# Optimization experiments

Hardware: AMD Instinct MI355X
Metric: run time of the kernel (lower is better)

The kernel has to match this reference:

```python
import jax, jax.numpy as jnp
import numpy as np

B, M, R = 1024, 2048, 8192  # batch of states, metabolites, reactions
SPARSITY = 0.002            # ~4 nonzero substrates / products per reaction


def setup_inputs() -> dict:
    key = jax.random.key(0)
    k1, k2, k3, k4, k5, k6 = jax.random.split(key, 6)
    # concentrations must be strictly positive (log used in power-law eval)
    conc = jax.random.uniform(k1, (B, M), minval=1e-3, maxval=1.0, dtype=jnp.float32)
    # sparse kinetic-order (exponent) matrix: ~4 substrates/reaction, order 1 or 2
    e_mask = jax.random.bernoulli(k2, SPARSITY, (M, R))
    E = jnp.where(e_mask, jax.random.randint(k3, (M, R), 1, 3), 0).astype(jnp.int32)
    # sparse stoichiometry matrix with coefficients in {-2,-1,1,2}
    s_mask = jax.random.bernoulli(k4, SPARSITY, (M, R))
    s_raw = jax.random.randint(k5, (M, R), 0, 4)
    s_val = jnp.where(s_raw < 2, s_raw - 2, s_raw - 1)  # {-2,-1,1,2}
    S = jnp.where(s_mask, s_val, 0).astype(jnp.int32)
    # per-reaction rate constants (the learned ParameterDict)
    k = jax.random.uniform(k6, (R,), minval=0.1, maxval=2.0, dtype=jnp.float32)
    return {"conc": conc, "E": E, "S": S, "k": k}


def reference(conc, E, S, k):
    # mass-action rate laws: v_j = k_j * prod_i c_i^{E_ij}, evaluated in log-space
    # logc: [B, M]; Ef: [M, R] -> v: [B, R]
    logc = jnp.log(conc)
    Ef = E.astype(conc.dtype)
    v = k * jnp.exp(jnp.einsum('bm,mr->br', logc, Ef))
    # stoichiometric ODE RHS: dX/dt = v @ S^T -> [B, M]
    Sf = S.astype(conc.dtype)
    dXdt = jnp.einsum('br,mr->bm', v, Sf)
    return dXdt
```

## Files before the change

### kernel.cpp

```cpp
#include <hip/hip_runtime.h>
#include <hip/hip_fp16.h>

#define Bsz 1024
#define Mm  2048
#define Rr  8192
#define EMAX 32
#define SMAX 64

typedef unsigned short ushort_t;

__global__ __launch_bounds__(256) void transpose_log(
    const float* __restrict__ conc, __half2* __restrict__ logcTh2,
    int* __restrict__ ecnt, unsigned int* __restrict__ elist32)
{
    const int g = blockIdx.x * 256 + threadIdx.x;
    if (g < Rr) ecnt[g] = 0;
    elist32[g] = 0;

    __shared__ float tile[64][65];
    const int mt = (blockIdx.x % (Mm / 64)) * 64;
    const int bt = (blockIdx.x / (Mm / 64)) * 64;
    const int lm = threadIdx.x & 63;
    const int w  = threadIdx.x >> 6;
    for (int i = w; i < 64; i += 4)
        tile[lm][i] = __logf(conc[(size_t)(bt + i) * Mm + mt + lm]);
    __syncthreads();
    for (int idx = threadIdx.x; idx < 64 * 32; idx += 256) {
        const int j  = idx >> 5;
        const int bp = idx & 31;
        logcTh2[((size_t)(mt + j) << 9) + (bt >> 1) + bp] =
            __floats2half2_rn(tile[j][2 * bp], tile[j][2 * bp + 1]);
    }
}

__global__ __launch_bounds__(256) void build_lists(
    const int* __restrict__ E, const int* __restrict__ S,
    int* __restrict__ ecnt, ushort_t* __restrict__ elist,
    int* __restrict__ scnt, ushort_t* __restrict__ slist)
{
    __shared__ int n_hits;
    __shared__ int buf[256];
    const int t = threadIdx.x;
    if (t == 0) n_hits = 0;
    __syncthreads();

    if (blockIdx.x < 2048) {
        const int m = blockIdx.x;
        const int4* E4 = (const int4*)E + (size_t)m * 2048;
        int4 e[8];
        #pragma unroll
        for (int u = 0; u < 8; ++u) e[u] = E4[t + 256 * u];
        #pragma unroll
        for (int u = 0; u < 8; ++u) {
            const int r0 = (t + 256 * u) << 2;
            int ev[4] = {e[u].x, e[u].y, e[u].z, e[u].w};
            #pragma unroll
            for (int q = 0; q < 4; ++q)
                if (ev[q]) {
                    int i = atomicAdd(&n_hits, 1);
                    if (i < 256) buf[i] = (ev[q] << 13) | (r0 + q);
                }
        }
        __syncthreads();
        const int en = min(n_hits, 256);
        if (t < en) {
            int wv = buf[t];
            int r  = wv & 0x1FFF;
            int ev = wv >> 13;
            int slot = atomicAdd(&ecnt[r], 1);
            if (slot < EMAX) elist[r * EMAX + slot] = (ushort_t)((ev << 11) | m);
        }
    } else {
        const int m = blockIdx.x - 2048;
        const int4* S4 = (const int4*)S + (size_t)m * 2048;
        int4 s[8];
        #pragma unroll
        for (int u = 0; u < 8; ++u) s[u] = S4[t + 256 * u];
        #pragma unroll
        for (int u = 0; u < 8; ++u) {
            const int r0 = (t + 256 * u) << 2;
            int sv[4] = {s[u].x, s[u].y, s[u].z, s[u].w};
            #pragma unroll
            for (int q = 0; q < 4; ++q)
                if (sv[q]) {
                    int i = atomicAdd(&n_hits, 1);
                    if (i < 256) buf[i] = ((sv[q] + 2) << 13) | (r0 + q);
                }
        }
        __syncthreads();
        const int sn = min(n_hits, SMAX);
        if (t == 0) scnt[m] = sn;
        if (t < SMAX)
            slist[m * SMAX + t] = (t < sn) ? (ushort_t)buf[t]
                                           : (ushort_t)0x4000;
    }
}

__global__ __launch_bounds__(256) void rates_kernel(
    const __half2* __restrict__ logcTh2, const float* __restrict__ kvec,
    const int* __restrict__ ecnt, const ushort_t* __restrict__ elist,
    __half2* __restrict__ VTh)
{
    const int rblk = blockIdx.x & 1023;
    const int bg   = blockIdx.x >> 10;
    const int b2   = bg * 256 + threadIdx.x;
    for (int rr = 0; rr < 8; ++rr) {
        const int r = rblk * 8 + rr;
        const ushort_t* row = elist + (r << 5);
        float2 s = make_float2(0.f, 0.f);
        unsigned w; float2 g;
        #define EGATHER(word)                                                  \
            w = (unsigned)(word);                                              \
            g = __half22float2(logcTh2[(size_t)((w & 0x7FF) << 9) + b2]);      \
            s.x += (float)((w & 0xFFFF) >> 11) * g.x;                          \
            s.y += (float)((w & 0xFFFF) >> 11) * g.y;                          \
            g = __half22float2(logcTh2[(size_t)(((w >> 16) & 0x7FF) << 9) + b2]); \
            s.x += (float)(w >> 27) * g.x;                                     \
            s.y += (float)(w >> 27) * g.y;
        int2 W = *(const int2*)(row);
        EGATHER(W.x) EGATHER(W.y)
        const int cnt = min(ecnt[r], EMAX);
        for (int j = 4; j < cnt; j += 4) {
            int2 T = *(const int2*)(row + j);
            EGATHER(T.x) EGATHER(T.y)
        }
        #undef EGATHER
        const float kk = kvec[r];
        VTh[((size_t)r << 9) + b2] =
            __floats2half2_rn(kk * __expf(s.x), kk * __expf(s.y));
    }
}

__global__ __launch_bounds__(256) void assemble_kernel(
    const __half2* __restrict__ VTh,
    const int* __restrict__ scnt, const ushort_t* __restrict__ slist,
    float* __restrict__ out)
{
    const int mblk = blockIdx.x & 511;
    const int bg   = blockIdx.x >> 9;
    const int b2   = bg * 256 + threadIdx.x;
    const int m0   = mblk * 4;
    float2 acc[4];
    #pragma unroll
    for (int mm = 0; mm < 4; ++mm) {
        const int m = m0 + mm;
        const ushort_t* row = slist + (m << 6);
        float2 a = make_float2(0.f, 0.f);
        unsigned w; float2 v; float sw;
        #define SGATHER(word)                                                  \
            w = (unsigned)(word);                                              \
            v = __half22float2(VTh[(size_t)((w & 0x1FFF) << 9) + b2]);         \
            sw = (float)((int)((w & 0xFFFF) >> 13) - 2);                       \
            a.x += sw * v.x;  a.y += sw * v.y;                                 \
            v = __half22float2(VTh[(size_t)(((w >> 16) & 0x1FFF) << 9) + b2]); \
            sw = (float)((int)(w >> 29) - 2);                                  \
            a.x += sw * v.x;  a.y += sw * v.y;
        int4 W0 = *(const int4*)(row);
        int4 W1 = *(const int4*)(row + 8);
        SGATHER(W0.x) SGATHER(W0.y) SGATHER(W0.z) SGATHER(W0.w)
        SGATHER(W1.x) SGATHER(W1.y) SGATHER(W1.z) SGATHER(W1.w)
        const int cnt = min(scnt[m], SMAX);
        for (int j = 16; j < cnt; j += 8) {
            int4 T = *(const int4*)(row + j);
            SGATHER(T.x) SGATHER(T.y) SGATHER(T.z) SGATHER(T.w)
        }
        #undef SGATHER
        acc[mm] = a;
    }
    const int b = 2 * b2;
    *(float4*)(out + (size_t)b * Mm + m0) =
        make_float4(acc[0].x, acc[1].x, acc[2].x, acc[3].x);
    *(float4*)(out + (size_t)(b + 1) * Mm + m0) =
        make_float4(acc[0].y, acc[1].y, acc[2].y, acc[3].y);
}

extern "C" void kernel_launch(void* const* d_in, const int* in_sizes, int n_in,
                              void* d_out, int out_size, void* d_ws, size_t ws_size,
                              hipStream_t stream) {
    const float* conc = (const float*)d_in[0];
    const int*   E    = (const int*)d_in[1];
    const int*   S    = (const int*)d_in[2];
    const float* kvec = (const float*)d_in[3];
    float* out = (float*)d_out;

    __half2* VTh     = (__half2*)d_ws;
    __half2* logcTh2 = (__half2*)((char*)d_ws + (size_t)Rr * Bsz * sizeof(__half));
    int*    ecnt     = (int*)((char*)logcTh2 + (size_t)Mm * Bsz * sizeof(__half));
    int*    scnt     = ecnt + Rr;
    ushort_t* elist  = (ushort_t*)(scnt + Mm);
    ushort_t* slist  = elist + Rr * EMAX;
    const size_t need = (size_t)Rr * Bsz * sizeof(__half)
                      + (size_t)Mm * Bsz * sizeof(__half)
                      + (size_t)(Rr + Mm) * sizeof(int)
                      + (size_t)(Rr * EMAX + Mm * SMAX) * sizeof(ushort_t);
    if (ws_size < need) return;

    transpose_log<<<512, 256, 0, stream>>>(conc, logcTh2, ecnt, (unsigned int*)elist);
    build_lists<<<4096, 256, 0, stream>>>(E, S, ecnt, elist, scnt, slist);
    rates_kernel<<<2048, 256, 0, stream>>>(logcTh2, kvec, ecnt, elist, VTh);
    assemble_kernel<<<1024, 256, 0, stream>>>(VTh, scnt, slist, out);
}
```

Baseline: 193.8 us.

## Split batch into eight slabs so each XCD gathers from one L2-resident slab

```diff
diff --git a/kernel.cpp b/kernel.cpp
--- a/kernel.cpp
+++ b/kernel.cpp
@@ -25,10 +25,13 @@
     for (int i = w; i < 64; i += 4)
         tile[lm][i] = __logf(conc[(size_t)(bt + i) * Mm + mt + lm]);
     __syncthreads();
+    const int s       = bt >> 7;
+    const int colbase = (bt & 127) >> 1;
+    __half2* dst = logcTh2 + (size_t)s * (Mm * 64);
     for (int idx = threadIdx.x; idx < 64 * 32; idx += 256) {
         const int j  = idx >> 5;
         const int bp = idx & 31;
-        logcTh2[((size_t)(mt + j) << 9) + (bt >> 1) + bp] =
+        dst[(mt + j) * 64 + colbase + bp] =
             __floats2half2_rn(tile[j][2 * bp], tile[j][2 * bp + 1]);
     }
 }
@@ -101,22 +104,25 @@
     const int* __restrict__ ecnt, const ushort_t* __restrict__ elist,
     __half2* __restrict__ VTh)
 {
-    const int rblk = blockIdx.x & 1023;
-    const int bg   = blockIdx.x >> 10;
-    const int b2   = bg * 256 + threadIdx.x;
-    for (int rr = 0; rr < 8; ++rr) {
-        const int r = rblk * 8 + rr;
+    const int s   = blockIdx.x & 7;
+    const int rch = blockIdx.x >> 3;
+    const int col = threadIdx.x & 63;
+    const int wr  = threadIdx.x >> 6;
+    const __half2* lc = logcTh2 + (size_t)s * (Mm * 64);
+    __half2* vt = VTh + (size_t)s * (Rr * 64);
+    unsigned w; float2 g;
+    #define EGATHER(word)                                                  \
+        w = (unsigned)(word);                                              \
+        g = __half22float2(lc[(w & 0x7FF) * 64 + col]);                    \
+        acc.x += (float)((w & 0xFFFF) >> 11) * g.x;                        \
+        acc.y += (float)((w & 0xFFFF) >> 11) * g.y;                        \
+        g = __half22float2(lc[((w >> 16) & 0x7FF) * 64 + col]);            \
+        acc.x += (float)(w >> 27) * g.x;                                   \
+        acc.y += (float)(w >> 27) * g.y;
+    for (int i = 0; i < 8; ++i) {
+        const int r = rch * 32 + i * 4 + wr;
         const ushort_t* row = elist + (r << 5);
-        float2 s = make_float2(0.f, 0.f);
-        unsigned w; float2 g;
-        #define EGATHER(word)                                                  \
-            w = (unsigned)(word);                                              \
-            g = __half22float2(logcTh2[(size_t)((w & 0x7FF) << 9) + b2]);      \
-            s.x += (float)((w & 0xFFFF) >> 11) * g.x;                          \
-            s.y += (float)((w & 0xFFFF) >> 11) * g.y;                          \
-            g = __half22float2(logcTh2[(size_t)(((w >> 16) & 0x7FF) << 9) + b2]); \
-            s.x += (float)(w >> 27) * g.x;                                     \
-            s.y += (float)(w >> 27) * g.y;
+        float2 acc = make_float2(0.f, 0.f);
         int2 W = *(const int2*)(row);
         EGATHER(W.x) EGATHER(W.y)
         const int cnt = min(ecnt[r], EMAX);
@@ -124,37 +130,37 @@
             int2 T = *(const int2*)(row + j);
             EGATHER(T.x) EGATHER(T.y)
         }
-        #undef EGATHER
         const float kk = kvec[r];
-        VTh[((size_t)r << 9) + b2] =
-            __floats2half2_rn(kk * __expf(s.x), kk * __expf(s.y));
-    }
+        vt[r * 64 + col] = __floats2half2_rn(kk * __expf(acc.x), kk * __expf(acc.y));
+    }
+    #undef EGATHER
 }
 
 __global__ __launch_bounds__(256) void assemble_kernel(
-    const __half2* __restrict__ VTh,
-    const int* __restrict__ scnt, const ushort_t* __restrict__ slist,
-    float* __restrict__ out)
-{
-    const int mblk = blockIdx.x & 511;
-    const int bg   = blockIdx.x >> 9;
-    const int b2   = bg * 256 + threadIdx.x;
-    const int m0   = mblk * 4;
-    float2 acc[4];
-    #pragma unroll
-    for (int mm = 0; mm < 4; ++mm) {
-        const int m = m0 + mm;
+    const __half2* __restrict__ VTh, const int* __restrict__ scnt,
+    const ushort_t* __restrict__ slist, float* __restrict__ out)
+{
+    __shared__ float tile[128][17];
+    const int s   = blockIdx.x & 7;
+    const int mch = blockIdx.x >> 3;
+    const int col = threadIdx.x & 63;
+    const int wm  = threadIdx.x >> 6;
+    const __half2* vt = VTh + (size_t)s * (Rr * 64);
+    const int m0 = mch * 16;
+    unsigned w; float2 v; float sw;
+    #define SGATHER(word)                                                  \
+        w = (unsigned)(word);                                              \
+        v = __half22float2(vt[(w & 0x1FFF) * 64 + col]);                   \
+        sw = (float)((int)((w & 0xFFFF) >> 13) - 2);                       \
+        a.x += sw * v.x;  a.y += sw * v.y;                                 \
+        v = __half22float2(vt[((w >> 16) & 0x1FFF) * 64 + col]);           \
+        sw = (float)((int)(w >> 29) - 2);                                  \
+        a.x += sw * v.x;  a.y += sw * v.y;
+    for (int i = 0; i < 4; ++i) {
+        const int ml = i * 4 + wm;
+        const int m  = m0 + ml;
         const ushort_t* row = slist + (m << 6);
         float2 a = make_float2(0.f, 0.f);
-        unsigned w; float2 v; float sw;
-        #define SGATHER(word)                                                  \
-            w = (unsigned)(word);                                              \
-            v = __half22float2(VTh[(size_t)((w & 0x1FFF) << 9) + b2]);         \
-            sw = (float)((int)((w & 0xFFFF) >> 13) - 2);                       \
-            a.x += sw * v.x;  a.y += sw * v.y;                                 \
-            v = __half22float2(VTh[(size_t)(((w >> 16) & 0x1FFF) << 9) + b2]); \
-            sw = (float)((int)(w >> 29) - 2);                                  \
-            a.x += sw * v.x;  a.y += sw * v.y;
         int4 W0 = *(const int4*)(row);
         int4 W1 = *(const int4*)(row + 8);
         SGATHER(W0.x) SGATHER(W0.y) SGATHER(W0.z) SGATHER(W0.w)
@@ -164,14 +170,18 @@
             int4 T = *(const int4*)(row + j);
             SGATHER(T.x) SGATHER(T.y) SGATHER(T.z) SGATHER(T.w)
         }
-        #undef SGATHER
-        acc[mm] = a;
-    }
-    const int b = 2 * b2;
-    *(float4*)(out + (size_t)b * Mm + m0) =
-        make_float4(acc[0].x, acc[1].x, acc[2].x, acc[3].x);
-    *(float4*)(out + (size_t)(b + 1) * Mm + m0) =
-        make_float4(acc[0].y, acc[1].y, acc[2].y, acc[3].y);
+        tile[2 * col][ml]     = a.x;
+        tile[2 * col + 1][ml] = a.y;
+    }
+    #undef SGATHER
+    __syncthreads();
+    #pragma unroll
+    for (int pass = 0; pass < 2; ++pass) {
+        const int bl = (threadIdx.x >> 2) + pass * 64;
+        const int fl = threadIdx.x & 3;
+        float4 vv = *(const float4*)&tile[bl][fl * 4];
+        *(float4*)(out + (size_t)(s * 128 + bl) * Mm + m0 + fl * 4) = vv;
+    }
 }
 
 extern "C" void kernel_launch(void* const* d_in, const int* in_sizes, int n_in,
```

Measured after the change: 193.1 us. Within noise of the previous version (-0.4%).
